# Performance work log

Measured on AMD Instinct MI355X. Metric: run time of the kernel, lower is better.

## Reference

```python
import jax, jax.numpy as jnp
from jax import lax
import numpy as np

VOCAB, E, H, T = 8000, 300, 75, 6  # H = hidden_dim//2 per direction
B, S = 256, 512
START, STOP = 4, 5
NEG = -10000.0


def setup_inputs() -> dict:
    key = jax.random.key(0)
    ks = jax.random.split(key, 16)
    sc = 0.1  # keep activations in sane range
    trans = jax.random.normal(ks[14], (T, T), jnp.float32)
    trans = trans.at[START, :].set(NEG).at[:, STOP].set(NEG)
    return {
        "sentence": jax.random.randint(ks[0], (B, S), 0, VOCAB),
        "tags": jax.random.randint(ks[1], (B, S), 0, 4),  # only B/I/E/S gold tags
        "embedding": jax.random.normal(ks[2], (VOCAB, E), jnp.float32),
        "w_ih_f": sc * jax.random.normal(ks[3], (4 * H, E), jnp.float32),
        "w_hh_f": sc * jax.random.normal(ks[4], (4 * H, H), jnp.float32),
        "b_ih_f": sc * jax.random.normal(ks[5], (4 * H,), jnp.float32),
        "b_hh_f": sc * jax.random.normal(ks[6], (4 * H,), jnp.float32),
        "w_ih_b": sc * jax.random.normal(ks[7], (4 * H, E), jnp.float32),
        "w_hh_b": sc * jax.random.normal(ks[8], (4 * H, H), jnp.float32),
        "b_ih_b": sc * jax.random.normal(ks[9], (4 * H,), jnp.float32),
        "b_hh_b": sc * jax.random.normal(ks[10], (4 * H,), jnp.float32),
        "h0": jax.random.normal(ks[11], (2, B, H), jnp.float32),
        "c0": jax.random.normal(ks[12], (2, B, H), jnp.float32),
        "w_out": sc * jax.random.normal(ks[13], (T, 2 * H), jnp.float32),
        "b_out": sc * jax.random.normal(ks[15], (T,), jnp.float32),
        "transitions": trans,
    }


def _lstm_dir(xg, w_hh, h0, c0, reverse):
    # xg: [S, B, 4H] precomputed input gates; PyTorch gate order i, f, g, o
    def step(carry, g):
        h, c = carry
        gates = g + h @ w_hh.T
        i, f, gg, o = jnp.split(gates, 4, axis=-1)
        c = jax.nn.sigmoid(f) * c + jax.nn.sigmoid(i) * jnp.tanh(gg)
        h = jax.nn.sigmoid(o) * jnp.tanh(c)
        return (h, c), h

    _, hs = lax.scan(step, (h0, c0), xg, reverse=reverse)
    return hs  # [S, B, H]


def reference(sentence, tags, embedding, w_ih_f, w_hh_f, b_ih_f, b_hh_f,
              w_ih_b, w_hh_b, b_ih_b, b_hh_b, h0, c0, w_out, b_out, transitions):
    # --- BiLSTM features ---
    embeds = embedding[sentence].transpose(1, 0, 2)  # [S, B, E]
    xg_f = embeds @ w_ih_f.T + (b_ih_f + b_hh_f)
    xg_b = embeds @ w_ih_b.T + (b_ih_b + b_hh_b)
    hf = _lstm_dir(xg_f, w_hh_f, h0[0], c0[0], reverse=False)
    hb = _lstm_dir(xg_b, w_hh_b, h0[1], c0[1], reverse=True)
    lstm_out = jnp.concatenate([hf, hb], axis=-1)  # [S, B, 2H]
    feats = lstm_out @ w_out.T + b_out  # [S, B, T]

    # --- CRF forward algorithm (log partition) ---
    alpha0 = jnp.full((feats.shape[1], T), NEG, feats.dtype).at[:, START].set(0.0)

    def crf_step(alpha, feat):
        # alpha_new[b, j] = logsumexp_i(alpha[b, i] + trans[j, i] + feat[b, j])
        alpha = jax.nn.logsumexp(
            alpha[:, None, :] + transitions[None, :, :] + feat[:, :, None], axis=2)
        return alpha, None

    alpha, _ = lax.scan(crf_step, alpha0, feats)
    forward_score = jax.nn.logsumexp(alpha + transitions[STOP][None, :], axis=1)  # [B]

    # --- gold path score ---
    tags_ext = jnp.concatenate(
        [jnp.full((tags.shape[0], 1), START, tags.dtype), tags], axis=1)  # [B, S+1]
    trans_sc = transitions[tags_ext[:, 1:], tags_ext[:, :-1]].sum(axis=1)  # [B]
    feats_bt = feats.transpose(1, 0, 2)  # [B, S, T]
    emit_sc = jnp.take_along_axis(feats_bt, tags[:, :, None], axis=2)[..., 0].sum(axis=1)
    gold_score = trans_sc + emit_sc + transitions[STOP, tags[:, -1]]

    return forward_score - gold_score  # [B] per-sentence CRF NLL
```

## Files before the change

kernel.cpp:

```cpp
#include <hip/hip_runtime.h>
#include <stdint.h>

#define VOCABN 8000
#define EE     300
#define HH     75
#define G4     300
#define TT     6
#define BB     256
#define SS     512
#define STARTT 4
#define STOPT  5
#define NEGV   (-10000.0f)
#define NCH    16
#define CHL    32

typedef __fp16 fp16x2 __attribute__((ext_vector_type(2)));
typedef __fp16 f16x8 __attribute__((ext_vector_type(8)));
typedef float f32x4 __attribute__((ext_vector_type(4)));
typedef unsigned int u32;

__device__ __forceinline__ float sigf(float x){
  return __builtin_amdgcn_rcpf(1.0f + __expf(-x));
}
__device__ __forceinline__ float tanhf_(float x){
  return __builtin_fmaf(__builtin_amdgcn_rcpf(1.0f + __expf(-2.0f * x)), 2.0f, -1.0f);
}
__device__ __forceinline__ float pk2(float a, float b){
  fp16x2 r = __builtin_amdgcn_cvt_pkrtz(a, b);
  return __builtin_bit_cast(float, r);
}
__device__ __forceinline__ float dot2pk(float a, float b, float c){
  asm("v_dot2_f32_f16 %0, %1, %2, %0" : "+v"(c) : "v"(a), "v"(b));
  return c;
}
__device__ __forceinline__ void sync_lds(){
  __builtin_amdgcn_sched_barrier(0);
  asm volatile("s_waitcnt lgkmcnt(0)" ::: "memory");
  __builtin_amdgcn_s_barrier();
  __builtin_amdgcn_sched_barrier(0);
}

#define LDSR 20
__global__ __launch_bounds__(256) void k_gemm(
    const float* __restrict__ emb, const float* __restrict__ w_ih_f,
    const float* __restrict__ w_ih_b,
    const float* __restrict__ b_ih_f, const float* __restrict__ b_hh_f,
    const float* __restrict__ b_ih_b, const float* __restrict__ b_hh_b,
    float* __restrict__ vxg){
  __shared__ alignas(16) float a_sh[128 * LDSR];
  __shared__ alignas(16) float b_sh[64 * LDSR];
  __shared__ float bias_sh[64];
  const int bx = blockIdx.x;
  const int dir = bx / (63 * 5);
  const int rem = bx % (63 * 5);
  const int vt = rem / 5, gt = rem % 5;
  const int v0 = vt * 128, g0 = gt * 64;
  const int tid = threadIdx.x;
  const float* wdir = dir ? w_ih_b : w_ih_f;

  if (tid < 64){
    int g = g0 + tid;
    float bi = 0.f;
    if (g < G4) bi = dir ? (b_ih_b[g] + b_hh_b[g]) : (b_ih_f[g] + b_hh_f[g]);
    bias_sh[tid] = bi;
  }

  float acc[8][4];
  #pragma unroll
  for (int i = 0; i < 8; ++i)
    #pragma unroll
    for (int j = 0; j < 4; ++j) acc[i][j] = 0.f;

  const int tx = tid & 15, ty = tid >> 4;
  const int la_r = tid >> 1, la_h = (tid & 1) * 8;
  const int lb_r = tid >> 2, lb_h = (tid & 3) * 4;

  const int va = v0 + la_r;
  const float* arow = emb + (size_t)(va < VOCABN ? va : 0) * EE;
  const int gb = g0 + lb_r;
  const float* brow = wdir + (size_t)(gb < G4 ? gb : 0) * EE;
  const float4 z4 = {0.f, 0.f, 0.f, 0.f};

  for (int kk = 0; kk < 19; ++kk){
    const int e0 = kk * 16;
    float4 av0 = *(const float4*)&arow[e0 + la_h];
    float4 av1 = (e0 + la_h + 7 < EE) ? *(const float4*)&arow[e0 + la_h + 4] : z4;
    float4 bv  = (e0 + lb_h + 3 < EE) ? *(const float4*)&brow[e0 + lb_h]     : z4;
    __syncthreads();
    *(float4*)&a_sh[la_r * LDSR + la_h]     = av0;
    *(float4*)&a_sh[la_r * LDSR + la_h + 4] = av1;
    *(float4*)&b_sh[lb_r * LDSR + lb_h]     = bv;
    __syncthreads();
    #pragma unroll
    for (int e4 = 0; e4 < 4; ++e4){
      float4 bq[4], aq[8];
      #pragma unroll
      for (int j = 0; j < 4; ++j) bq[j] = *(const float4*)&b_sh[(tx + 16 * j) * LDSR + e4 * 4];
      #pragma unroll
      for (int i = 0; i < 8; ++i) aq[i] = *(const float4*)&a_sh[(ty + 16 * i) * LDSR + e4 * 4];
      #pragma unroll
      for (int i = 0; i < 8; ++i)
        #pragma unroll
        for (int j = 0; j < 4; ++j)
          acc[i][j] += aq[i].x * bq[j].x + aq[i].y * bq[j].y
                     + aq[i].z * bq[j].z + aq[i].w * bq[j].w;
    }
  }

  const size_t obase = (size_t)dir * VOCABN * G4;
  #pragma unroll
  for (int i = 0; i < 8; ++i){
    int v = v0 + ty + 16 * i;
    if (v < VOCABN){
      #pragma unroll
      for (int j = 0; j < 4; ++j){
        int g = g0 + tx + 16 * j;
        if (g < G4){
          int gp = 4 * (g % 75) + (g / 75);
          vxg[obase + (size_t)v * G4 + gp] = acc[i][j] + bias_sh[tx + 16 * j];
        }
      }
    }
  }
}

__global__ __launch_bounds__(640) void k_lstm(
    const int* __restrict__ sentence, const float* __restrict__ vxg,
    const float* __restrict__ w_hh_f, const float* __restrict__ w_hh_b,
    const float* __restrict__ h0, const float* __restrict__ c0,
    const float* __restrict__ w_out, const float* __restrict__ b_out,
    float* __restrict__ featsF, float* __restrict__ featsB){
  __shared__ int tok_sh[SS * 16];
  __shared__ alignas(16) __fp16 hfrag[2][12 * 16 * 8];
  const int bx = blockIdx.x;
  const int dir = bx >> 4, group = bx & 15;
  const int t = threadIdx.x;
  const int w = t >> 6, lane = t & 63;
  const int bb = lane & 15, q = lane >> 4;
  const int T0 = 2 * w, T1 = 2 * w + 1;
  const int rbA = 16 * T0 + 4 * q, rbB = 16 * T1 + 4 * q;
  const int hA = rbA >> 2, hB = rbB >> 2;
  const int bglob = group * 16 + bb;
  const int wiA = w * 128 + bb * 8 + q;
  const int wiB = w * 128 + bb * 8 + 4 + q;

  for (int i = t; i < 2 * 12 * 16 * 4; i += 640) ((u32*)hfrag)[i] = 0;
  for (int i = t; i < 16 * SS; i += 640){
    int bq = i >> 9, s = i & 511;
    tok_sh[s * 16 + ((bq + s) & 15)] = sentence[(size_t)(group * 16 + bq) * SS + s];
  }
  __syncthreads();

  const float* whh = dir ? w_hh_b : w_hh_f;
  f16x8 a00, a01, a02, a10, a11, a12;
  #define BUILD_A(dst, T, c) { \
    int m = 16 * (T) + bb; int kb = 32 * (c) + 8 * q; \
    _Pragma("unroll") \
    for (int j = 0; j < 8; ++j){ \
      int kk = kb + j; float wv = 0.f; \
      if (kk < HH){ \
        if (m < 300) wv = whh[((m & 3) * 75 + (m >> 2)) * HH + kk]; \
        else if (m < 306) wv = w_out[(m - 300) * (2 * HH) + dir * HH + kk]; \
      } \
      dst[j] = (__fp16)wv; } }
  BUILD_A(a00, T0, 0) BUILD_A(a01, T0, 1) BUILD_A(a02, T0, 2)
  BUILD_A(a10, T1, 0) BUILD_A(a11, T1, 1) BUILD_A(a12, T1, 2)

  float cA = 0.f, cB = 0.f;
  if (hA < HH){
    cA = c0[((size_t)dir * BB + bglob) * HH + hA];
    hfrag[0][wiA] = (__fp16)h0[((size_t)dir * BB + bglob) * HH + hA];
  }
  if (hB < HH){
    cB = c0[((size_t)dir * BB + bglob) * HH + hB];
    hfrag[0][wiB] = (__fp16)h0[((size_t)dir * BB + bglob) * HH + hB];
  }
  const float bo0 = dir ? 0.f : b_out[0], bo1 = dir ? 0.f : b_out[1];
  const float bo2 = dir ? 0.f : b_out[2], bo3 = dir ? 0.f : b_out[3];
  const float bo4 = dir ? 0.f : b_out[4], bo5 = dir ? 0.f : b_out[5];
  __syncthreads();

  const float* vx = vxg + (size_t)dir * VOCABN * G4;
  float* feats = dir ? featsB : featsF;
  const float4 zf4 = {0.f, 0.f, 0.f, 0.f};

  float4 cur0 = zf4, cur1 = zf4, nx0 = zf4, nx1 = zf4;
  {
    int p = dir ? (SS - 1) : 0;
    int tk = tok_sh[p * 16 + ((bb + p) & 15)];
    const float* base = vx + (size_t)tk * G4;
    if (hA < HH) cur0 = *(const float4*)(base + rbA);
    if (hB < HH) cur1 = *(const float4*)(base + rbB);
    p = dir ? (SS - 2) : 1;
    tk = tok_sh[p * 16 + ((bb + p) & 15)];
    base = vx + (size_t)tk * G4;
    if (hA < HH) nx0 = *(const float4*)(base + rbA);
    if (hB < HH) nx1 = *(const float4*)(base + rbB);
  }

  for (int k = 0; k <= SS; ++k){
    const __fp16* hq = hfrag[k & 1];
    f16x8 b0 = *(const f16x8*)&hq[(0 * 64 + lane) * 8];
    f16x8 b1 = *(const f16x8*)&hq[(1 * 64 + lane) * 8];
    f16x8 b2 = *(const f16x8*)&hq[(2 * 64 + lane) * 8];

    float4 p0 = zf4, p1 = zf4;
    if (k + 2 < SS){
      int p = dir ? (SS - 3 - k) : (k + 2);
      int tk = tok_sh[p * 16 + ((bb + p) & 15)];
      const float* base = vx + (size_t)tk * G4;
      if (hA < HH) p0 = *(const float4*)(base + rbA);
      if (hB < HH) p1 = *(const float4*)(base + rbB);
    }

    f32x4 acc0 = {0.f, 0.f, 0.f, 0.f}, acc1 = {0.f, 0.f, 0.f, 0.f};
    asm("v_mfma_f32_16x16x32_f16 %0, %1, %2, %0" : "+v"(acc0) : "a"(a00), "v"(b0));
    asm("v_mfma_f32_16x16x32_f16 %0, %1, %2, %0" : "+v"(acc1) : "a"(a10), "v"(b0));
    asm("v_mfma_f32_16x16x32_f16 %0, %1, %2, %0" : "+v"(acc0) : "a"(a01), "v"(b1));
    asm("v_mfma_f32_16x16x32_f16 %0, %1, %2, %0" : "+v"(acc1) : "a"(a11), "v"(b1));
    asm("v_mfma_f32_16x16x32_f16 %0, %1, %2, %0" : "+v"(acc0) : "a"(a02), "v"(b2));
    asm("v_mfma_f32_16x16x32_f16 %0, %1, %2, %0" : "+v"(acc1) : "a"(a12), "v"(b2));

    __fp16* hw = hfrag[(k & 1) ^ 1];
    if (k < SS){
      if (hA < HH){
        float gi = acc0.x + cur0.x, gf = acc0.y + cur0.y;
        float gg = acc0.z + cur0.z, go = acc0.w + cur0.w;
        cA = sigf(gf) * cA + sigf(gi) * tanhf_(gg);
        hw[wiA] = (__fp16)(sigf(go) * tanhf_(cA));
      }
      if (hB < HH){
        float gi = acc1.x + cur1.x, gf = acc1.y + cur1.y;
        float gg = acc1.z + cur1.z, go = acc1.w + cur1.w;
        cB = sigf(gf) * cB + sigf(gi) * tanhf_(gg);
        hw[wiB] = (__fp16)(sigf(go) * tanhf_(cB));
      }
    }
    if (k >= 1){
      if (rbA == 300){
        int ps = dir ? (SS - k) : (k - 1);
        float* fb = feats + ((size_t)ps * BB + bglob) * TT;
        float2 v01 = {acc0.x + bo0, acc0.y + bo1};
        float2 v23 = {acc0.z + bo2, acc0.w + bo3};
        *(float2*)fb = v01;
        *(float2*)(fb + 2) = v23;
      }
      if (rbB == 304){
        int ps = dir ? (SS - k) : (k - 1);
        float* fb = feats + ((size_t)ps * BB + bglob) * TT;
        float2 v45 = {acc1.x + bo4, acc1.y + bo5};
        *(float2*)(fb + 4) = v45;
      }
    }
    cur0 = nx0; cur1 = nx1; nx0 = p0; nx1 = p1;
    sync_lds();
  }
}

#define LOADSTAGE(X0,X1,X2,Y0,Y1,Y2, srow) do{ \
  int _r = (srow); if (_r >= SS) _r = 0; \
  const float2* _pF = (const float2*)(featsF + ((size_t)_r * BB + b) * TT); \
  const float2* _pB = (const float2*)(featsB + ((size_t)_r * BB + b) * TT); \
  X0 = _pF[0]; X1 = _pF[1]; X2 = _pF[2]; \
  Y0 = _pB[0]; Y1 = _pB[1]; Y2 = _pB[2]; }while(0)

#define ASTEP(X0,X1,X2,Y0,Y1,Y2, srow) do{ \
  float F0 = X0.x + Y0.x, F1 = X0.y + Y0.y, F2 = X1.x + Y1.x; \
  float F3 = X1.y + Y1.y, F4 = X2.x + Y2.x, F5 = X2.y + Y2.y; \
  float M = fmaxf(fmaxf(fmaxf(a0,a1),fmaxf(a2,a3)),fmaxf(a4,a5)); \
  float p01 = pk2(__expf(a0-M), __expf(a1-M)); \
  float p23 = pk2(__expf(a2-M), __expf(a3-M)); \
  float p45 = pk2(__expf(a4-M), __expf(a5-M)); \
  float s0 = dot2pk(p45, Tq2,  dot2pk(p23, Tq1,  dot2pk(p01, Tq0,  0.f))); \
  float s1 = dot2pk(p45, Tq5,  dot2pk(p23, Tq4,  dot2pk(p01, Tq3,  0.f))); \
  float s2 = dot2pk(p45, Tq8,  dot2pk(p23, Tq7,  dot2pk(p01, Tq6,  0.f))); \
  float s3 = dot2pk(p45, Tq11, dot2pk(p23, Tq10, dot2pk(p01, Tq9,  0.f))); \
  float s4 = dot2pk(p45, Tq14, dot2pk(p23, Tq13, dot2pk(p01, Tq12, 0.f))); \
  float s5 = dot2pk(p45, Tq17, dot2pk(p23, Tq16, dot2pk(p01, Tq15, 0.f))); \
  a0 = M + __logf(fmaxf(s0, 1e-37f)) + F0;  a1 = M + __logf(fmaxf(s1, 1e-37f)) + F1; \
  a2 = M + __logf(fmaxf(s2, 1e-37f)) + F2;  a3 = M + __logf(fmaxf(s3, 1e-37f)) + F3; \
  a4 = M + __logf(fmaxf(s4, 1e-37f)) + F4;  a5 = M + __logf(fmaxf(s5, 1e-37f)) + F5; \
  LOADSTAGE(X0,X1,X2,Y0,Y1,Y2, (srow) + 2); }while(0)

__global__ __launch_bounds__(256) void k_crf_scan(
    const float* __restrict__ featsF, const float* __restrict__ featsB,
    const float* __restrict__ trans, const int* __restrict__ tags,
    float* __restrict__ crfM, float* __restrict__ pgold){
  __shared__ float tr_sh[36];
  __shared__ u32 etp_sh[18];
  const int tid = threadIdx.x;
  if (tid < 36) tr_sh[tid] = trans[tid];
  if (tid < 18) etp_sh[tid] = __float_as_uint(
      pk2(__expf(trans[2 * tid]), __expf(trans[2 * tid + 1])));
  __syncthreads();
  const int bx = blockIdx.x;

  if (bx < 96){
    const int g = bx * 256 + tid;
    const int s0i = g % 6;
    const int c = (g / 6) % NCH;
    const int b = g / (6 * NCH);
    const int cbase = c * CHL;

    float Tq0=__int_as_float(etp_sh[0]),  Tq1=__int_as_float(etp_sh[1]),
          Tq2=__int_as_float(etp_sh[2]),  Tq3=__int_as_float(etp_sh[3]),
          Tq4=__int_as_float(etp_sh[4]),  Tq5=__int_as_float(etp_sh[5]),
          Tq6=__int_as_float(etp_sh[6]),  Tq7=__int_as_float(etp_sh[7]),
          Tq8=__int_as_float(etp_sh[8]),  Tq9=__int_as_float(etp_sh[9]),
          Tq10=__int_as_float(etp_sh[10]), Tq11=__int_as_float(etp_sh[11]),
          Tq12=__int_as_float(etp_sh[12]), Tq13=__int_as_float(etp_sh[13]),
          Tq14=__int_as_float(etp_sh[14]), Tq15=__int_as_float(etp_sh[15]),
          Tq16=__int_as_float(etp_sh[16]), Tq17=__int_as_float(etp_sh[17]);

    float a0 = (s0i == 0) ? 0.f : NEGV, a1 = (s0i == 1) ? 0.f : NEGV;
    float a2 = (s0i == 2) ? 0.f : NEGV, a3 = (s0i == 3) ? 0.f : NEGV;
    float a4 = (s0i == 4) ? 0.f : NEGV, a5 = (s0i == 5) ? 0.f : NEGV;

    float2 xA0,xA1,xA2,yA0,yA1,yA2, xB0,xB1,xB2,yB0,yB1,yB2;
    LOADSTAGE(xA0,xA1,xA2,yA0,yA1,yA2, cbase + 0);
    LOADSTAGE(xB0,xB1,xB2,yB0,yB1,yB2, cbase + 1);
    for (int s = 0; s < CHL; s += 2){
      ASTEP(xA0,xA1,xA2,yA0,yA1,yA2, cbase + s);
      ASTEP(xB0,xB1,xB2,yB0,yB1,yB2, cbase + s + 1);
    }
    float* mrow = crfM + ((size_t)(b * NCH + c) * 6 + s0i) * 6;
    mrow[0] = a0; mrow[1] = a1; mrow[2] = a2;
    mrow[3] = a3; mrow[4] = a4; mrow[5] = a5;
  } else {
    const int g2 = (bx - 96) * 256 + tid;
    const int b = g2 / NCH;
    const int c = g2 % NCH;
    const int* tg = tags + (size_t)b * SS + c * CHL;
    int prev = (c == 0) ? STARTT : tg[-1];
    float acc = 0.f;
    #pragma unroll 4
    for (int s = 0; s < CHL; ++s){
      int ct = tg[s];
      size_t fo = (size_t)(c * CHL + s) * BB * TT + (size_t)b * TT + ct;
      acc += tr_sh[ct * 6 + prev] + featsF[fo] + featsB[fo];
      prev = ct;
    }
    pgold[b * NCH + c] = acc;
  }
}

__global__ __launch_bounds__(64) void k_crf_comb(
    const float* __restrict__ crfM, const float* __restrict__ pgold,
    const float* __restrict__ trans, const int* __restrict__ tags,
    float* __restrict__ out){
  const int b = blockIdx.x * 64 + threadIdx.x;
  float v0 = NEGV, v1 = NEGV, v2 = NEGV, v3 = NEGV, v4 = 0.f, v5 = NEGV;
  for (int c = 0; c < NCH; ++c){
    const float* mb = crfM + (size_t)(b * NCH + c) * 36;
    float n[6];
    #pragma unroll
    for (int j = 0; j < 6; ++j){
      float t0 = v0 + mb[0 * 6 + j], t1 = v1 + mb[1 * 6 + j];
      float t2 = v2 + mb[2 * 6 + j], t3 = v3 + mb[3 * 6 + j];
      float t4 = v4 + mb[4 * 6 + j], t5 = v5 + mb[5 * 6 + j];
      float m = fmaxf(fmaxf(fmaxf(t0,t1),fmaxf(t2,t3)),fmaxf(t4,t5));
      float s = __expf(t0-m)+__expf(t1-m)+__expf(t2-m)
              + __expf(t3-m)+__expf(t4-m)+__expf(t5-m);
      n[j] = m + __logf(s);
    }
    v0 = n[0]; v1 = n[1]; v2 = n[2]; v3 = n[3]; v4 = n[4]; v5 = n[5];
  }
  float z0 = v0 + trans[30], z1 = v1 + trans[31], z2 = v2 + trans[32];
  float z3 = v3 + trans[33], z4 = v4 + trans[34], z5 = v5 + trans[35];
  float M2 = fmaxf(fmaxf(fmaxf(z0,z1),fmaxf(z2,z3)),fmaxf(z4,z5));
  float ss = __expf(z0-M2)+__expf(z1-M2)+__expf(z2-M2)
           + __expf(z3-M2)+__expf(z4-M2)+__expf(z5-M2);
  float fwd = M2 + __logf(ss);

  float gold = trans[STOPT * 6 + tags[(size_t)b * SS + SS - 1]];
  #pragma unroll
  for (int c = 0; c < NCH; ++c) gold += pgold[b * NCH + c];
  out[b] = fwd - gold;
}

extern "C" void kernel_launch(void* const* d_in, const int* in_sizes, int n_in,
                              void* d_out, int out_size, void* d_ws, size_t ws_size,
                              hipStream_t stream){
  const int*   sentence = (const int*)  d_in[0];
  const int*   tags     = (const int*)  d_in[1];
  const float* emb      = (const float*)d_in[2];
  const float* w_ih_f   = (const float*)d_in[3];
  const float* w_hh_f   = (const float*)d_in[4];
  const float* b_ih_f   = (const float*)d_in[5];
  const float* b_hh_f   = (const float*)d_in[6];
  const float* w_ih_b   = (const float*)d_in[7];
  const float* w_hh_b   = (const float*)d_in[8];
  const float* b_ih_b   = (const float*)d_in[9];
  const float* b_hh_b   = (const float*)d_in[10];
  const float* h0       = (const float*)d_in[11];
  const float* c0       = (const float*)d_in[12];
  const float* w_out    = (const float*)d_in[13];
  const float* b_out    = (const float*)d_in[14];
  const float* trans    = (const float*)d_in[15];
  float* out = (float*)d_out;

  float* ws = (float*)d_ws;
  float* vxg    = ws;
  float* featsF = vxg + (size_t)2 * VOCABN * G4;
  float* featsB = featsF + (size_t)SS * BB * TT;
  float* crfM   = featsB + (size_t)SS * BB * TT;
  float* pgold  = crfM + (size_t)BB * NCH * 36;

  k_gemm<<<2 * 63 * 5, 256, 0, stream>>>(emb, w_ih_f, w_ih_b,
                                         b_ih_f, b_hh_f, b_ih_b, b_hh_b, vxg);
  k_lstm<<<32, 640, 0, stream>>>(sentence, vxg, w_hh_f, w_hh_b, h0, c0, w_out, b_out,
                                 featsF, featsB);
  k_crf_scan<<<96 + 16, 256, 0, stream>>>(featsF, featsB, trans, tags, crfM, pgold);
  k_crf_comb<<<BB / 64, 64, 0, stream>>>(crfM, pgold, trans, tags, out);
}
```

Before: 529.3 us.

## Shrink LSTM recurrence block to four waves with five MFMA tiles each

The recurrent LSTM kernel now runs each block with 4 waves of 256 threads instead of 10 waves of 640, and each wave handles five 16-row gate tiles instead of two. Fewer waves per block should make the per-step LDS barrier cheaper across the 512-step serial recurrence. Token storage in LDS is narrowed to 16-bit, and the GEMM writes gates in the order the LSTM reads them by permuting its weight rows and biases on input instead of scattering the output. In exchange each wave does more serial MFMA and activation work per step and holds more registers.

```diff
diff --git a/kernel.cpp b/kernel.cpp
--- a/kernel.cpp
+++ b/kernel.cpp
@@ -18,6 +18,7 @@
 typedef __fp16 f16x8 __attribute__((ext_vector_type(8)));
 typedef float f32x4 __attribute__((ext_vector_type(4)));
 typedef unsigned int u32;
+typedef unsigned short u16;
 
 __device__ __forceinline__ float sigf(float x){
   return __builtin_amdgcn_rcpf(1.0f + __expf(-x));
@@ -61,7 +62,10 @@
   if (tid < 64){
     int g = g0 + tid;
     float bi = 0.f;
-    if (g < G4) bi = dir ? (b_ih_b[g] + b_hh_b[g]) : (b_ih_f[g] + b_hh_f[g]);
+    if (g < G4){
+      int gs = (g & 3) * 75 + (g >> 2);
+      bi = dir ? (b_ih_b[gs] + b_hh_b[gs]) : (b_ih_f[gs] + b_hh_f[gs]);
+    }
     bias_sh[tid] = bi;
   }
 
@@ -78,7 +82,8 @@
   const int va = v0 + la_r;
   const float* arow = emb + (size_t)(va < VOCABN ? va : 0) * EE;
   const int gb = g0 + lb_r;
-  const float* brow = wdir + (size_t)(gb < G4 ? gb : 0) * EE;
+  const int gsrc = (gb & 3) * 75 + (gb >> 2);
+  const float* brow = wdir + (size_t)(gb < G4 ? gsrc : 0) * EE;
   const float4 z4 = {0.f, 0.f, 0.f, 0.f};
 
   for (int kk = 0; kk < 19; ++kk){
@@ -115,66 +120,68 @@
       #pragma unroll
       for (int j = 0; j < 4; ++j){
         int g = g0 + tx + 16 * j;
-        if (g < G4){
-          int gp = 4 * (g % 75) + (g / 75);
-          vxg[obase + (size_t)v * G4 + gp] = acc[i][j] + bias_sh[tx + 16 * j];
-        }
+        if (g < G4) vxg[obase + (size_t)v * G4 + g] = acc[i][j] + bias_sh[tx + 16 * j];
       }
     }
   }
 }
 
-__global__ __launch_bounds__(640) void k_lstm(
+#define TILE_LIST(F) F(0) F(1) F(2) F(3) F(4)
+
+__global__ __launch_bounds__(256) void k_lstm(
     const int* __restrict__ sentence, const float* __restrict__ vxg,
     const float* __restrict__ w_hh_f, const float* __restrict__ w_hh_b,
     const float* __restrict__ h0, const float* __restrict__ c0,
     const float* __restrict__ w_out, const float* __restrict__ b_out,
     float* __restrict__ featsF, float* __restrict__ featsB){
-  __shared__ int tok_sh[SS * 16];
+  __shared__ u16 tok_sh[SS * 16];
   __shared__ alignas(16) __fp16 hfrag[2][12 * 16 * 8];
   const int bx = blockIdx.x;
   const int dir = bx >> 4, group = bx & 15;
   const int t = threadIdx.x;
   const int w = t >> 6, lane = t & 63;
   const int bb = lane & 15, q = lane >> 4;
-  const int T0 = 2 * w, T1 = 2 * w + 1;
-  const int rbA = 16 * T0 + 4 * q, rbB = 16 * T1 + 4 * q;
-  const int hA = rbA >> 2, hB = rbB >> 2;
   const int bglob = group * 16 + bb;
-  const int wiA = w * 128 + bb * 8 + q;
-  const int wiB = w * 128 + bb * 8 + 4 + q;
-
-  for (int i = t; i < 2 * 12 * 16 * 4; i += 640) ((u32*)hfrag)[i] = 0;
-  for (int i = t; i < 16 * SS; i += 640){
+
+  for (int i = t; i < 2 * 12 * 16 * 4; i += 256) ((u32*)hfrag)[i] = 0;
+  for (int i = t; i < 16 * SS; i += 256){
     int bq = i >> 9, s = i & 511;
-    tok_sh[s * 16 + ((bq + s) & 15)] = sentence[(size_t)(group * 16 + bq) * SS + s];
+    tok_sh[s * 16 + ((bq + s) & 15)] =
+        (u16)sentence[(size_t)(group * 16 + bq) * SS + s];
   }
   __syncthreads();
 
   const float* whh = dir ? w_hh_b : w_hh_f;
-  f16x8 a00, a01, a02, a10, a11, a12;
-  #define BUILD_A(dst, T, c) { \
-    int m = 16 * (T) + bb; int kb = 32 * (c) + 8 * q; \
+
+#define DECL_T(U) \
+  const int hv##U = 20 * w + 4 * U + q; \
+  const int rb##U = 80 * w + 16 * U + 4 * q; \
+  const int wi##U = (hv##U >> 3) * 128 + bb * 8 + (hv##U & 7); \
+  f16x8 a##U##_0, a##U##_1, a##U##_2; \
+  float cell##U = 0.f;
+  TILE_LIST(DECL_T)
+
+#define FILL_A(U) { \
+    int m = 16 * (5 * w + U) + bb; \
     _Pragma("unroll") \
-    for (int j = 0; j < 8; ++j){ \
-      int kk = kb + j; float wv = 0.f; \
-      if (kk < HH){ \
-        if (m < 300) wv = whh[((m & 3) * 75 + (m >> 2)) * HH + kk]; \
-        else if (m < 306) wv = w_out[(m - 300) * (2 * HH) + dir * HH + kk]; \
-      } \
-      dst[j] = (__fp16)wv; } }
-  BUILD_A(a00, T0, 0) BUILD_A(a01, T0, 1) BUILD_A(a02, T0, 2)
-  BUILD_A(a10, T1, 0) BUILD_A(a11, T1, 1) BUILD_A(a12, T1, 2)
-
-  float cA = 0.f, cB = 0.f;
-  if (hA < HH){
-    cA = c0[((size_t)dir * BB + bglob) * HH + hA];
-    hfrag[0][wiA] = (__fp16)h0[((size_t)dir * BB + bglob) * HH + hA];
-  }
-  if (hB < HH){
-    cB = c0[((size_t)dir * BB + bglob) * HH + hB];
-    hfrag[0][wiB] = (__fp16)h0[((size_t)dir * BB + bglob) * HH + hB];
-  }
+    for (int c = 0; c < 3; ++c){ \
+      f16x8 tmp; \
+      _Pragma("unroll") \
+      for (int j = 0; j < 8; ++j){ \
+        int kk = 32 * c + 8 * q + j; float wv = 0.f; \
+        if (kk < HH){ \
+          if (m < 300) wv = whh[((m & 3) * 75 + (m >> 2)) * HH + kk]; \
+          else if (m < 306) wv = w_out[(m - 300) * (2 * HH) + dir * HH + kk]; \
+        } \
+        tmp[j] = (__fp16)wv; } \
+      if (c == 0) a##U##_0 = tmp; else if (c == 1) a##U##_1 = tmp; else a##U##_2 = tmp; } }
+  TILE_LIST(FILL_A)
+
+#define INIT_HC(U) if (hv##U < HH){ \
+    cell##U = c0[((size_t)dir * BB + bglob) * HH + hv##U]; \
+    hfrag[0][wi##U] = (__fp16)h0[((size_t)dir * BB + bglob) * HH + hv##U]; }
+  TILE_LIST(INIT_HC)
+
   const float bo0 = dir ? 0.f : b_out[0], bo1 = dir ? 0.f : b_out[1];
   const float bo2 = dir ? 0.f : b_out[2], bo3 = dir ? 0.f : b_out[3];
   const float bo4 = dir ? 0.f : b_out[4], bo5 = dir ? 0.f : b_out[5];
@@ -184,19 +191,18 @@
   float* feats = dir ? featsB : featsF;
   const float4 zf4 = {0.f, 0.f, 0.f, 0.f};
 
-  float4 cur0 = zf4, cur1 = zf4, nx0 = zf4, nx1 = zf4;
-  {
-    int p = dir ? (SS - 1) : 0;
-    int tk = tok_sh[p * 16 + ((bb + p) & 15)];
-    const float* base = vx + (size_t)tk * G4;
-    if (hA < HH) cur0 = *(const float4*)(base + rbA);
-    if (hB < HH) cur1 = *(const float4*)(base + rbB);
-    p = dir ? (SS - 2) : 1;
-    tk = tok_sh[p * 16 + ((bb + p) & 15)];
-    base = vx + (size_t)tk * G4;
-    if (hA < HH) nx0 = *(const float4*)(base + rbA);
-    if (hB < HH) nx1 = *(const float4*)(base + rbB);
-  }
+#define SROW(kk) (dir ? (SS - 1 - (kk)) : (kk))
+#define LOADXG(dst, U, kstep) { \
+    if (hv##U < HH && (kstep) < SS){ \
+      int sr_ = SROW(kstep); \
+      int tk_ = tok_sh[sr_ * 16 + ((bb + sr_) & 15)]; \
+      dst = *(const float4*)(vx + (size_t)tk_ * G4 + rb##U); \
+    } else dst = zf4; }
+
+#define DECL_PF(U) float4 cur##U, nx##U, pf##U;
+  TILE_LIST(DECL_PF)
+#define INIT_PF(U) LOADXG(cur##U, U, 0) LOADXG(nx##U, U, 1)
+  TILE_LIST(INIT_PF)
 
   for (int k = 0; k <= SS; ++k){
     const __fp16* hq = hfrag[k & 1];
@@ -204,55 +210,41 @@
     f16x8 b1 = *(const f16x8*)&hq[(1 * 64 + lane) * 8];
     f16x8 b2 = *(const f16x8*)&hq[(2 * 64 + lane) * 8];
 
-    float4 p0 = zf4, p1 = zf4;
-    if (k + 2 < SS){
-      int p = dir ? (SS - 3 - k) : (k + 2);
-      int tk = tok_sh[p * 16 + ((bb + p) & 15)];
-      const float* base = vx + (size_t)tk * G4;
-      if (hA < HH) p0 = *(const float4*)(base + rbA);
-      if (hB < HH) p1 = *(const float4*)(base + rbB);
-    }
-
-    f32x4 acc0 = {0.f, 0.f, 0.f, 0.f}, acc1 = {0.f, 0.f, 0.f, 0.f};
-    asm("v_mfma_f32_16x16x32_f16 %0, %1, %2, %0" : "+v"(acc0) : "a"(a00), "v"(b0));
-    asm("v_mfma_f32_16x16x32_f16 %0, %1, %2, %0" : "+v"(acc1) : "a"(a10), "v"(b0));
-    asm("v_mfma_f32_16x16x32_f16 %0, %1, %2, %0" : "+v"(acc0) : "a"(a01), "v"(b1));
-    asm("v_mfma_f32_16x16x32_f16 %0, %1, %2, %0" : "+v"(acc1) : "a"(a11), "v"(b1));
-    asm("v_mfma_f32_16x16x32_f16 %0, %1, %2, %0" : "+v"(acc0) : "a"(a02), "v"(b2));
-    asm("v_mfma_f32_16x16x32_f16 %0, %1, %2, %0" : "+v"(acc1) : "a"(a12), "v"(b2));
+#define PREF(U) LOADXG(pf##U, U, k + 2)
+    TILE_LIST(PREF)
+
+#define MFMA_T(U) \
+    f32x4 acc##U = {0.f, 0.f, 0.f, 0.f}; \
+    asm("v_mfma_f32_16x16x32_f16 %0, %1, %2, %0" : "+v"(acc##U) : "a"(a##U##_0), "v"(b0)); \
+    asm("v_mfma_f32_16x16x32_f16 %0, %1, %2, %0" : "+v"(acc##U) : "a"(a##U##_1), "v"(b1)); \
+    asm("v_mfma_f32_16x16x32_f16 %0, %1, %2, %0" : "+v"(acc##U) : "a"(a##U##_2), "v"(b2));
+    TILE_LIST(MFMA_T)
 
     __fp16* hw = hfrag[(k & 1) ^ 1];
     if (k < SS){
-      if (hA < HH){
-        float gi = acc0.x + cur0.x, gf = acc0.y + cur0.y;
-        float gg = acc0.z + cur0.z, go = acc0.w + cur0.w;
-        cA = sigf(gf) * cA + sigf(gi) * tanhf_(gg);
-        hw[wiA] = (__fp16)(sigf(go) * tanhf_(cA));
-      }
-      if (hB < HH){
-        float gi = acc1.x + cur1.x, gf = acc1.y + cur1.y;
-        float gg = acc1.z + cur1.z, go = acc1.w + cur1.w;
-        cB = sigf(gf) * cB + sigf(gi) * tanhf_(gg);
-        hw[wiB] = (__fp16)(sigf(go) * tanhf_(cB));
-      }
-    }
-    if (k >= 1){
-      if (rbA == 300){
-        int ps = dir ? (SS - k) : (k - 1);
-        float* fb = feats + ((size_t)ps * BB + bglob) * TT;
-        float2 v01 = {acc0.x + bo0, acc0.y + bo1};
-        float2 v23 = {acc0.z + bo2, acc0.w + bo3};
+#define ACT(U) if (hv##U < HH){ \
+      float gi = acc##U.x + cur##U.x, gf = acc##U.y + cur##U.y; \
+      float gg = acc##U.z + cur##U.z, go = acc##U.w + cur##U.w; \
+      cell##U = sigf(gf) * cell##U + sigf(gi) * tanhf_(gg); \
+      hw[wi##U] = (__fp16)(sigf(go) * tanhf_(cell##U)); }
+      TILE_LIST(ACT)
+    }
+    if (k >= 1 && w == 3){
+      int ps = dir ? (SS - k) : (k - 1);
+      float* fb = feats + ((size_t)ps * BB + bglob) * TT;
+      if (q == 3){
+        float2 v01 = {acc3.x + bo0, acc3.y + bo1};
+        float2 v23 = {acc3.z + bo2, acc3.w + bo3};
         *(float2*)fb = v01;
         *(float2*)(fb + 2) = v23;
       }
-      if (rbB == 304){
-        int ps = dir ? (SS - k) : (k - 1);
-        float* fb = feats + ((size_t)ps * BB + bglob) * TT;
-        float2 v45 = {acc1.x + bo4, acc1.y + bo5};
+      if (q == 0){
+        float2 v45 = {acc4.x + bo4, acc4.y + bo5};
         *(float2*)(fb + 4) = v45;
       }
     }
-    cur0 = nx0; cur1 = nx1; nx0 = p0; nx1 = p1;
+#define ROT(U) cur##U = nx##U; nx##U = pf##U;
+    TILE_LIST(ROT)
     sync_lds();
   }
 }
@@ -408,7 +400,7 @@
 
   k_gemm<<<2 * 63 * 5, 256, 0, stream>>>(emb, w_ih_f, w_ih_b,
                                          b_ih_f, b_hh_f, b_ih_b, b_hh_b, vxg);
-  k_lstm<<<32, 640, 0, stream>>>(sentence, vxg, w_hh_f, w_hh_b, h0, c0, w_out, b_out,
+  k_lstm<<<32, 256, 0, stream>>>(sentence, vxg, w_hh_f, w_hh_b, h0, c0, w_out, b_out,
                                  featsF, featsB);
   k_crf_scan<<<96 + 16, 256, 0, stream>>>(featsF, featsB, trans, tags, crfM, pgold);
   k_crf_comb<<<BB / 64, 64, 0, stream>>>(crfM, pgold, trans, tags, out);
```

Result: slower. 685.0 us (+29.4%).
